# Kernel tuning notes

Hardware: AMD Instinct MI355X
Metric: run time of the kernel (lower is better)

The kernel has to match this reference:

```python
import jax, jax.numpy as jnp
import numpy as np

B, L, K, S, D, H, C = 32, 256, 50, 16, 128, 4, 128
V, NN, NU, NS = 50000, 100000, 50000, 5000


def mha(q, k, v, in_w, in_b, out_w, out_b, n_heads):
    # PyTorch nn.MultiheadAttention (batch_first, eval mode) semantics.
    d = q.shape[-1]
    hd = d // n_heads
    wq, wk, wv = jnp.split(in_w, 3, axis=0)
    bq, bk, bv = jnp.split(in_b, 3)
    def heads(t):
        return t.reshape(t.shape[:-1] + (n_heads, hd))
    qh = heads(q @ wq.T + bq)
    kh = heads(k @ wk.T + bk)
    vh = heads(v @ wv.T + bv)
    scores = jnp.einsum('...qhd,...khd->...hqk', qh, kh) / jnp.sqrt(jnp.asarray(hd, q.dtype))
    attn = jax.nn.softmax(scores, axis=-1)
    o = jnp.einsum('...hqk,...khd->...qhd', attn, vh)
    o = o.reshape(o.shape[:-2] + (d,))
    return o @ out_w.T + out_b


def conv1d(x, w, b):
    # x: [B, D, L], w: [Cout, D, k]
    y = jax.lax.conv_general_dilated(x, w, (1,), 'VALID', dimension_numbers=('NCH', 'OIH', 'NCH'))
    return y + b[None, :, None]


def meta_path_module(paths, gru_wih, gru_whh, gru_bih, gru_bhh, in_w, in_b, out_w, out_b, ln_g, ln_b):
    # paths: [B, S, T, D] -> [B, D]
    b, s, t, d = paths.shape
    x = paths.reshape(b * s, t, d)
    def step(h, xt):
        gi = xt @ gru_wih.T + gru_bih
        gh = h @ gru_whh.T + gru_bhh
        ir, iz, inn = jnp.split(gi, 3, axis=-1)
        hr, hz, hn = jnp.split(gh, 3, axis=-1)
        r = jax.nn.sigmoid(ir + hr)
        z = jax.nn.sigmoid(iz + hz)
        n = jnp.tanh(inn + r * hn)
        return (1.0 - z) * n + z * h, None
    h0 = jnp.zeros((b * s, d), paths.dtype)
    h, _ = jax.lax.scan(step, h0, jnp.swapaxes(x, 0, 1))
    enc = h.reshape(b, s, d)
    attn = mha(enc, enc, enc, in_w, in_b, out_w, out_b, H)
    y = enc + attn
    mu = jnp.mean(y, -1, keepdims=True)
    var = jnp.var(y, -1, keepdims=True)
    y = (y - mu) / jnp.sqrt(var + 1e-5) * ln_g + ln_b
    return jnp.mean(y, axis=1)


def _forward(word_table, news_table, user_table, source_table,
             wa_in_w, wa_in_b, wa_out_w, wa_out_b,
             conv_w3, conv_b3, conv_w4, conv_b4, conv_w5, conv_b5, fc_w, fc_b,
             nsn_gru_wih, nsn_gru_whh, nsn_gru_bih, nsn_gru_bhh,
             nsn_in_w, nsn_in_b, nsn_out_w, nsn_out_b, nsn_ln_g, nsn_ln_b,
             nun_gru_wih, nun_gru_whh, nun_gru_bih, nun_gru_bhh,
             nun_in_w, nun_in_b, nun_out_w, nun_out_b, nun_ln_g, nun_ln_b,
             mp_w1, mp_b1, mp_w2, mp_b2, cls_w1, cls_b1, cls_w2, cls_b2,
             news_ids, news_word_indices, word_ctx_ids, nsn_src, nsn_end, nun_usr, nun_end):
    # --- fine-grained word embeds: per-token query attending over context news ---
    base = word_table[news_word_indices]              # [B, L, D]
    ctx = news_table[word_ctx_ids]                    # [B, L, K, D] (dominant gather)
    q = base[:, :, None, :]                           # [B, L, 1, D]
    fine = mha(q, ctx, ctx, wa_in_w, wa_in_b, wa_out_w, wa_out_b, H)[:, :, 0, :]
    pad = (news_word_indices == 0)[..., None]
    doc = jnp.where(pad, jnp.zeros((), base.dtype), fine)   # padding_idx=0 -> zeros
    # --- coarse CNN encoder ---
    x = jnp.swapaxes(doc, 1, 2)                       # [B, D, L]
    pooled = [jnp.max(jax.nn.relu(conv1d(x, w, b)), axis=2)
              for w, b in ((conv_w3, conv_b3), (conv_w4, conv_b4), (conv_w5, conv_b5))]
    semantic = jnp.concatenate(pooled, axis=1) @ fc_w.T + fc_b   # [B, D]
    # --- meta-path interaction ---
    start = jnp.broadcast_to(news_table[news_ids][:, None, :], (B, S, D))
    nsn_paths = jnp.stack([start, source_table[nsn_src], news_table[nsn_end]], axis=2)
    nun_paths = jnp.stack([start, user_table[nun_usr], news_table[nun_end]], axis=2)
    nsn_e = meta_path_module(nsn_paths, nsn_gru_wih, nsn_gru_whh, nsn_gru_bih, nsn_gru_bhh,
                             nsn_in_w, nsn_in_b, nsn_out_w, nsn_out_b, nsn_ln_g, nsn_ln_b)
    nun_e = meta_path_module(nun_paths, nun_gru_wih, nun_gru_whh, nun_gru_bih, nun_gru_bhh,
                             nun_in_w, nun_in_b, nun_out_w, nun_out_b, nun_ln_g, nun_ln_b)
    stack = jnp.stack([nsn_e, nun_e], axis=1)         # [B, 2, D]
    sc = jnp.tanh(stack @ mp_w1.T + mp_b1) @ mp_w2.T + mp_b2
    w = jax.nn.softmax(sc, axis=1)
    struct = jnp.sum(stack * w, axis=1)
    comb = jnp.concatenate([semantic, struct], axis=1)
    hcls = jax.nn.relu(comb @ cls_w1.T + cls_b1)
    return hcls @ cls_w2.T + cls_b2                   # [B, 2]


def setup_inputs() -> dict:
    key = jax.random.key(0)
    ks = iter(jax.random.split(key, 80))
    def p(shape):
        return (jax.random.normal(next(ks), shape, jnp.float32) * 0.02)
    inp = {}
    inp['news_ids'] = jax.random.randint(next(ks), (B,), 0, NN)
    inp['news_word_indices'] = jax.random.randint(next(ks), (B, L), 0, V)
    inp['word_ctx_ids'] = jax.random.randint(next(ks), (B, L, K), 0, NN)
    inp['nsn_src'] = jax.random.randint(next(ks), (B, S), 0, NS)
    inp['nsn_end'] = jax.random.randint(next(ks), (B, S), 0, NN)
    inp['nun_usr'] = jax.random.randint(next(ks), (B, S), 0, NU)
    inp['nun_end'] = jax.random.randint(next(ks), (B, S), 0, NN)
    inp['word_table'] = p((V, D)).at[0].set(0.0)
    inp['news_table'] = p((NN, D))
    inp['user_table'] = p((NU, D))
    inp['source_table'] = p((NS, D))
    inp['wa_in_w'] = p((3 * D, D)); inp['wa_in_b'] = p((3 * D,))
    inp['wa_out_w'] = p((D, D)); inp['wa_out_b'] = p((D,))
    for k in (3, 4, 5):
        inp[f'conv_w{k}'] = p((C, D, k)); inp[f'conv_b{k}'] = p((C,))
    inp['fc_w'] = p((D, 3 * C)); inp['fc_b'] = p((D,))
    for pre in ('nsn', 'nun'):
        inp[f'{pre}_gru_wih'] = p((3 * D, D)); inp[f'{pre}_gru_whh'] = p((3 * D, D))
        inp[f'{pre}_gru_bih'] = p((3 * D,)); inp[f'{pre}_gru_bhh'] = p((3 * D,))
        inp[f'{pre}_in_w'] = p((3 * D, D)); inp[f'{pre}_in_b'] = p((3 * D,))
        inp[f'{pre}_out_w'] = p((D, D)); inp[f'{pre}_out_b'] = p((D,))
        inp[f'{pre}_ln_g'] = jnp.ones((D,), jnp.float32); inp[f'{pre}_ln_b'] = jnp.zeros((D,), jnp.float32)
    inp['mp_w1'] = p((D // 2, D)); inp['mp_b1'] = p((D // 2,))
    inp['mp_w2'] = p((1, D // 2)); inp['mp_b2'] = p((1,))
    inp['cls_w1'] = p((D, 2 * D)); inp['cls_b1'] = p((D,))
    inp['cls_w2'] = p((2, D)); inp['cls_b2'] = p((2,))
    return inp


def reference(word_table, news_table, user_table, source_table,
              wa_in_w, wa_in_b, wa_out_w, wa_out_b,
              conv_w3, conv_b3, conv_w4, conv_b4, conv_w5, conv_b5, fc_w, fc_b,
              nsn_gru_wih, nsn_gru_whh, nsn_gru_bih, nsn_gru_bhh,
              nsn_in_w, nsn_in_b, nsn_out_w, nsn_out_b, nsn_ln_g, nsn_ln_b,
              nun_gru_wih, nun_gru_whh, nun_gru_bih, nun_gru_bhh,
              nun_in_w, nun_in_b, nun_out_w, nun_out_b, nun_ln_g, nun_ln_b,
              mp_w1, mp_b1, mp_w2, mp_b2, cls_w1, cls_b1, cls_w2, cls_b2,
              news_ids, news_word_indices, word_ctx_ids, nsn_src, nsn_end, nun_usr, nun_end):
    return _forward(word_table, news_table, user_table, source_table,
                    wa_in_w, wa_in_b, wa_out_w, wa_out_b,
                    conv_w3, conv_b3, conv_w4, conv_b4, conv_w5, conv_b5, fc_w, fc_b,
                    nsn_gru_wih, nsn_gru_whh, nsn_gru_bih, nsn_gru_bhh,
                    nsn_in_w, nsn_in_b, nsn_out_w, nsn_out_b, nsn_ln_g, nsn_ln_b,
                    nun_gru_wih, nun_gru_whh, nun_gru_bih, nun_gru_bhh,
                    nun_in_w, nun_in_b, nun_out_w, nun_out_b, nun_ln_g, nun_ln_b,
                    mp_w1, mp_b1, mp_w2, mp_b2, cls_w1, cls_b1, cls_w2, cls_b2,
                    news_ids, news_word_indices, word_ctx_ids, nsn_src, nsn_end, nun_usr, nun_end)
```

## Files before the change

### kernel.cpp

```cpp
#include <hip/hip_runtime.h>
#include <hip/hip_bf16.h>

#define BB 32
#define LL 256
#define KC 50
#define SS 16
#define DD 128
#define NH 4
#define CC 128
#define VV 50000
#define NNN 100000
#define NUU 50000
#define NSS 5000

typedef __attribute__((ext_vector_type(8))) short bf16x8;
typedef __attribute__((ext_vector_type(8))) unsigned short u16x8;
typedef __attribute__((ext_vector_type(4))) float f32x4;

#define APAD 132

__device__ __forceinline__ float dot4(float4 a, float4 b){
  return a.x*b.x + a.y*b.y + a.z*b.z + a.w*b.w;
}

__device__ __forceinline__ unsigned short f2bf(float f){
  union { float f; unsigned int u; } v; v.f = f;
  unsigned int r = (v.u + 0x7FFFu + ((v.u >> 16) & 1u)) >> 16;
  return (unsigned short)r;
}
__device__ __forceinline__ float bf2f(unsigned short s){
  union { unsigned int u; float f; } v; v.u = ((unsigned int)s) << 16;
  return v.f;
}

__global__ __launch_bounds__(256) void k_prep(
    const float* __restrict__ w3, const float* __restrict__ w4,
    const float* __restrict__ w5,
    const float* __restrict__ wih0, const float* __restrict__ whh0,
    const float* __restrict__ wih1, const float* __restrict__ whh1,
    const float* __restrict__ in_w, const float* __restrict__ out_w,
    unsigned short* __restrict__ wb3, unsigned short* __restrict__ wb4,
    unsigned short* __restrict__ wb5, unsigned short* __restrict__ wgb,
    unsigned short* __restrict__ wab){
  int e = blockIdx.x*256 + threadIdx.x;
  if (e < CC*DD*3){ int c=e/(DD*3), rm=e%(DD*3), d=rm/3, jj=rm%3;
    wb3[((size_t)jj*CC + c)*DD + d] = f2bf(w3[e]); }
  if (e < CC*DD*4){ int c=e/(DD*4), rm=e%(DD*4), d=rm/4, jj=rm%4;
    wb4[((size_t)jj*CC + c)*DD + d] = f2bf(w4[e]); }
  if (e < CC*DD*5){ int c=e/(DD*5), rm=e%(DD*5), d=rm/5, jj=rm%5;
    wb5[((size_t)jj*CC + c)*DD + d] = f2bf(w5[e]); }
  if (e < 384*DD){
    wgb[e]          = f2bf(wih0[e]);
    wgb[49152 + e]  = f2bf(whh0[e]);
    wgb[98304 + e]  = f2bf(wih1[e]);
    wgb[147456 + e] = f2bf(whh1[e]);
    wab[e]          = f2bf(in_w[e]);
  }
  if (e >= 384*DD && e < 512*DD) wab[e] = f2bf(out_w[e - 384*DD]);
}

__global__ __launch_bounds__(256) void k_projkv(
    const float* __restrict__ news, const unsigned short* __restrict__ wkvb,
    const float* __restrict__ in_b, unsigned short* __restrict__ nK,
    unsigned short* __restrict__ nV){
  __shared__ __align__(16) unsigned short Ts[64*APAD];
  const int tid = threadIdx.x;
  const int r0 = blockIdx.x * 64;
  for (int i = tid; i < 64*32; i += 256){
    int row = i >> 5, j = i & 31;
    int gr = r0 + row;
    float4 v = (gr < NNN) ? ((const float4*)(news + (size_t)gr*DD))[j]
                          : make_float4(0.f,0.f,0.f,0.f);
    unsigned short* d = Ts + row*APAD + j*4;
    d[0]=f2bf(v.x); d[1]=f2bf(v.y); d[2]=f2bf(v.z); d[3]=f2bf(v.w);
  }
  __syncthreads();
  const int wave = tid >> 6;
  const int lane = tid & 63;
  const int l15  = lane & 15;
  const int quad = lane >> 4;
  bf16x8 afr[4][4];
  #pragma unroll
  for (int mt=0; mt<4; mt++)
    #pragma unroll
    for (int ks=0; ks<4; ks++)
      afr[mt][ks] = *(const bf16x8*)(Ts + (mt*16 + l15)*APAD + ks*32 + quad*8);
  __syncthreads();
  for (int pass=0; pass<2; pass++){
    unsigned short* outp = pass ? nV : nK;
    #pragma unroll
    for (int t=0; t<2; t++){
      const int n0 = wave*32 + t*16;
      bf16x8 bfr[4];
      #pragma unroll
      for (int ks=0; ks<4; ks++)
        bfr[ks] = *(const bf16x8*)(wkvb + (size_t)(pass*128 + n0 + l15)*DD + ks*32 + quad*8);
      const float bias = in_b[128 + pass*128 + n0 + l15];
      #pragma unroll
      for (int mt=0; mt<4; mt++){
        f32x4 acc = {0.f,0.f,0.f,0.f};
        #pragma unroll
        for (int ks=0; ks<4; ks++)
          acc = __builtin_amdgcn_mfma_f32_16x16x32_bf16(afr[mt][ks], bfr[ks], acc, 0,0,0);
        const int col = n0 + l15;
        const int rb  = mt*16 + quad*4;
        #pragma unroll
        for (int r=0;r<4;r++)
          Ts[(rb + r)*APAD + col] = f2bf(acc[r] + bias);
      }
    }
    __syncthreads();
    for (int c = tid; c < 64*32; c += 256){
      int row = c >> 5, col4 = (c & 31) * 4;
      int gr = r0 + row;
      if (gr < NNN)
        *(unsigned long long*)(outp + (size_t)gr*128 + col4) =
            *(const unsigned long long*)(Ts + row*APAD + col4);
    }
    __syncthreads();
  }
}

__global__ __launch_bounds__(256) void k_qh(
    const float* __restrict__ word_table, const int* __restrict__ widx,
    const unsigned short* __restrict__ wqb, const float* __restrict__ in_b,
    float* __restrict__ qh){
  __shared__ __align__(16) unsigned short As[64*APAD];
  __shared__ int idx[64];
  const int tid = threadIdx.x;
  const int p0 = blockIdx.x * 64;
  if (tid < 64) idx[tid] = widx[p0 + tid];
  __syncthreads();
  for (int i = tid; i < 64*32; i += 256){
    int row = i >> 5, j = i & 31;
    float4 v = ((const float4*)(word_table + (size_t)idx[row]*DD))[j];
    unsigned short* d = As + row*APAD + j*4;
    d[0]=f2bf(v.x); d[1]=f2bf(v.y); d[2]=f2bf(v.z); d[3]=f2bf(v.w);
  }
  __syncthreads();
  const int wave = tid >> 6;
  const int lane = tid & 63;
  const int l15  = lane & 15;
  const int quad = lane >> 4;
  bf16x8 afr[4][4];
  #pragma unroll
  for (int mt=0; mt<4; mt++)
    #pragma unroll
    for (int ks=0; ks<4; ks++)
      afr[mt][ks] = *(const bf16x8*)(As + (mt*16 + l15)*APAD + ks*32 + quad*8);
  #pragma unroll
  for (int nt=0; nt<2; nt++){
    const int n0 = wave*32 + nt*16;
    bf16x8 bfr[4];
    #pragma unroll
    for (int ks=0; ks<4; ks++)
      bfr[ks] = *(const bf16x8*)(wqb + (size_t)(n0+l15)*DD + ks*32 + quad*8);
    const float bias = in_b[n0 + l15];
    #pragma unroll
    for (int mt=0; mt<4; mt++){
      f32x4 acc = {0.f,0.f,0.f,0.f};
      #pragma unroll
      for (int ks=0; ks<4; ks++)
        acc = __builtin_amdgcn_mfma_f32_16x16x32_bf16(afr[mt][ks], bfr[ks], acc, 0,0,0);
      #pragma unroll
      for (int r=0;r<4;r++){
        int m = mt*16 + quad*4 + r;
        qh[(size_t)(p0+m)*DD + n0 + l15] = acc[r] + bias;
      }
    }
  }
}

__global__ __launch_bounds__(64) void k_attn(
    const float* __restrict__ qh, const unsigned short* __restrict__ nK,
    const unsigned short* __restrict__ nV, const int* __restrict__ ctx_ids,
    float* __restrict__ o_out){
  const int p = blockIdx.x;
  const int lane = threadIdx.x;
  const int r = lane >> 4;
  const int g = lane & 15;
  const int h = g >> 2;
  __shared__ int ids[52];
  __shared__ float sc[NH][52];
  if (lane < KC) ids[lane] = ctx_ids[(size_t)p*KC + lane];
  float qv[8];
  {
    const float4* qp = (const float4*)(qh + (size_t)p*DD + g*8);
    float4 q0 = qp[0], q1 = qp[1];
    qv[0]=q0.x; qv[1]=q0.y; qv[2]=q0.z; qv[3]=q0.w;
    qv[4]=q1.x; qv[5]=q1.y; qv[6]=q1.z; qv[7]=q1.w;
  }
  __syncthreads();
  for (int kb=0; kb<13; kb++){
    int k2 = kb*4 + r;
    int row = ids[(k2 < KC) ? k2 : 0];
    u16x8 kv = *(const u16x8*)(nK + (size_t)row*DD + g*8);
    float pr = 0.f;
    #pragma unroll
    for (int j=0;j<8;j++) pr += qv[j]*bf2f(kv[j]);
    pr += __shfl_xor(pr, 1, 64);
    pr += __shfl_xor(pr, 2, 64);
    if ((g & 3) == 0 && k2 < KC) sc[h][k2] = pr;
  }
  __syncthreads();
  {
    const int hh = lane >> 4, kc = lane & 15;
    const float scale = 0.17677669529663687f;
    float mx = -1e30f;
    #pragma unroll
    for (int q4=0;q4<4;q4++){ int k2=kc+q4*16; if (k2<KC) mx = fmaxf(mx, sc[hh][k2]); }
    mx = fmaxf(mx, __shfl_xor(mx, 1, 64));
    mx = fmaxf(mx, __shfl_xor(mx, 2, 64));
    mx = fmaxf(mx, __shfl_xor(mx, 4, 64));
    mx = fmaxf(mx, __shfl_xor(mx, 8, 64));
    float sm = 0.f;
    float ev[4];
    #pragma unroll
    for (int q4=0;q4<4;q4++){
      int k2=kc+q4*16;
      ev[q4] = (k2<KC) ? __expf((sc[hh][k2]-mx)*scale) : 0.f;
      sm += ev[q4];
    }
    sm += __shfl_xor(sm, 1, 64);
    sm += __shfl_xor(sm, 2, 64);
    sm += __shfl_xor(sm, 4, 64);
    sm += __shfl_xor(sm, 8, 64);
    float inv = 1.f/sm;
    #pragma unroll
    for (int q4=0;q4<4;q4++){ int k2=kc+q4*16; if (k2<KC) sc[hh][k2] = ev[q4]*inv; }
  }
  __syncthreads();
  float acc[8];
  #pragma unroll
  for (int j=0;j<8;j++) acc[j]=0.f;
  for (int kb=0; kb<13; kb++){
    int k2 = kb*4 + r;
    int row = ids[(k2 < KC) ? k2 : 0];
    float w = (k2 < KC) ? sc[h][k2] : 0.f;
    u16x8 vv = *(const u16x8*)(nV + (size_t)row*DD + g*8);
    #pragma unroll
    for (int j=0;j<8;j++) acc[j] += w*bf2f(vv[j]);
  }
  #pragma unroll
  for (int j=0;j<8;j++){
    acc[j] += __shfl_xor(acc[j], 16, 64);
    acc[j] += __shfl_xor(acc[j], 32, 64);
  }
  if (r == 0){
    float4* op = (float4*)(o_out + (size_t)p*DD + g*8);
    op[0] = make_float4(acc[0],acc[1],acc[2],acc[3]);
    op[1] = make_float4(acc[4],acc[5],acc[6],acc[7]);
  }
}

__global__ __launch_bounds__(256) void k_wo(
    const float* __restrict__ o_attn, const int* __restrict__ widx,
    const unsigned short* __restrict__ wob, const float* __restrict__ out_b,
    float* __restrict__ doc){
  __shared__ __align__(16) unsigned short As[64*APAD];
  __shared__ int wm[64];
  const int tid = threadIdx.x;
  const int p0 = blockIdx.x * 64;
  if (tid < 64) wm[tid] = widx[p0 + tid];
  for (int i = tid; i < 64*32; i += 256){
    int row = i >> 5, j = i & 31;
    float4 v = ((const float4*)(o_attn + (size_t)(p0+row)*DD))[j];
    unsigned short* d = As + row*APAD + j*4;
    d[0]=f2bf(v.x); d[1]=f2bf(v.y); d[2]=f2bf(v.z); d[3]=f2bf(v.w);
  }
  __syncthreads();
  const int wave = tid >> 6;
  const int lane = tid & 63;
  const int l15  = lane & 15;
  const int quad = lane >> 4;
  bf16x8 afr[4][4];
  #pragma unroll
  for (int mt=0; mt<4; mt++)
    #pragma unroll
    for (int ks=0; ks<4; ks++)
      afr[mt][ks] = *(const bf16x8*)(As + (mt*16 + l15)*APAD + ks*32 + quad*8);
  #pragma unroll
  for (int nt=0; nt<2; nt++){
    const int n0 = wave*32 + nt*16;
    bf16x8 bfr[4];
    #pragma unroll
    for (int ks=0; ks<4; ks++)
      bfr[ks] = *(const bf16x8*)(wob + (size_t)(n0+l15)*DD + ks*32 + quad*8);
    const float bias = out_b[n0 + l15];
    #pragma unroll
    for (int mt=0; mt<4; mt++){
      f32x4 acc = {0.f,0.f,0.f,0.f};
      #pragma unroll
      for (int ks=0; ks<4; ks++)
        acc = __builtin_amdgcn_mfma_f32_16x16x32_bf16(afr[mt][ks], bfr[ks], acc, 0,0,0);
      #pragma unroll
      for (int r=0;r<4;r++){
        int m = mt*16 + quad*4 + r;
        doc[(size_t)(p0+m)*DD + n0 + l15] = (wm[m] == 0) ? 0.0f : (acc[r] + bias);
      }
    }
  }
}

#define CROWS 68
#define CPAD 136
__global__ __launch_bounds__(256) void k_conv(
    const float* __restrict__ doc, const unsigned short* __restrict__ wb3,
    const unsigned short* __restrict__ wb4, const unsigned short* __restrict__ wb5,
    float* __restrict__ convp){
  __shared__ __align__(16) char smem[CROWS*CPAD*2];
  unsigned short* ds = (unsigned short*)smem;
  float* smf = (float*)smem;
  const int blk = blockIdx.x;
  const int chunk = blk & 3;
  const int j = (blk >> 2) % 3;
  const int b = blk / 12;
  const int kk = 3 + j;
  const int T = LL - kk + 1;
  const int t0 = chunk * 64;
  const int nrows = 64 + kk - 1;
  const unsigned short* wb = (j==0) ? wb3 : (j==1) ? wb4 : wb5;
  const int tid = threadIdx.x;
  for (int i = tid; i < nrows*32; i += 256){
    int row = i >> 5, q4 = i & 31;
    int gt = t0 + row;
    float4 v = (gt < LL) ? ((const float4*)(doc + ((size_t)b*LL + gt)*DD))[q4]
                         : make_float4(0.f,0.f,0.f,0.f);
    unsigned short* dp = ds + row*CPAD + q4*4;
    dp[0]=f2bf(v.x); dp[1]=f2bf(v.y); dp[2]=f2bf(v.z); dp[3]=f2bf(v.w);
  }
  __syncthreads();
  const int wave = tid >> 6;
  const int lane = tid & 63;
  const int l15  = lane & 15;
  const int quad = lane >> 4;
  f32x4 acc[8];
  #pragma unroll
  for (int nt=0;nt<8;nt++) acc[nt] = (f32x4){0.f,0.f,0.f,0.f};
  for (int jj=0; jj<kk; jj++){
    #pragma unroll
    for (int ks=0; ks<4; ks++){
      bf16x8 af = *(const bf16x8*)(ds + (wave*16 + l15 + jj)*CPAD + ks*32 + quad*8);
      #pragma unroll
      for (int nt=0; nt<8; nt++){
        bf16x8 bf = *(const bf16x8*)(wb + ((size_t)jj*CC + nt*16 + l15)*DD + ks*32 + quad*8);
        acc[nt] = __builtin_amdgcn_mfma_f32_16x16x32_bf16(af, bf, acc[nt], 0,0,0);
      }
    }
  }
  __syncthreads();
  #pragma unroll
  for (int nt=0; nt<8; nt++){
    float mx = -1e30f;
    #pragma unroll
    for (int r=0;r<4;r++){
      int t = t0 + wave*16 + quad*4 + r;
      mx = fmaxf(mx, (t < T) ? acc[nt][r] : -1e30f);
    }
    mx = fmaxf(mx, __shfl_xor(mx, 16, 64));
    mx = fmaxf(mx, __shfl_xor(mx, 32, 64));
    if (quad == 0) smf[wave*128 + nt*16 + l15] = mx;
  }
  __syncthreads();
  if (tid < 128){
    float m4 = fmaxf(fmaxf(smf[tid], smf[128+tid]), fmaxf(smf[256+tid], smf[384+tid]));
    convp[(((size_t)b*3 + j)*4 + chunk)*CC + tid] = m4;
  }
}

#define GSTR 392
__global__ __launch_bounds__(256) void k_gru(
    const float* __restrict__ news_table, const float* __restrict__ user_table,
    const float* __restrict__ source_table,
    const int* __restrict__ news_ids, const int* __restrict__ nsn_src,
    const int* __restrict__ nsn_end, const int* __restrict__ nun_usr,
    const int* __restrict__ nun_end,
    const unsigned short* __restrict__ wgb,
    const float* __restrict__ bih0, const float* __restrict__ bhh0,
    const float* __restrict__ bih1, const float* __restrict__ bhh1,
    float* __restrict__ enc){
  __shared__ __align__(16) unsigned short xs[16][CPAD];
  __shared__ __align__(16) unsigned short hs[16][CPAD];
  __shared__ float hf[8][128];
  __shared__ float gi[8][GSTR];
  __shared__ float gh[8][GSTR];
  const int blk = blockIdx.x;
  const int m  = blk >> 6;
  const int b  = (blk >> 1) & 31;
  const int s0 = (blk & 1) * 8;
  const int tid = threadIdx.x;
  const int wave = tid >> 6, lane = tid & 63, l15 = lane & 15, quad = lane >> 4;
  const unsigned short* Wih = wgb + (size_t)m*2*384*DD;
  const unsigned short* Whh = Wih + 384*DD;
  const float* bih = m ? bih1 : bih0;
  const float* bhh = m ? bhh1 : bhh0;
  for (int i=tid;i<16*CPAD;i+=256){ (&xs[0][0])[i]=0; (&hs[0][0])[i]=0; }
  for (int i=tid;i<8*128;i+=256) (&hf[0][0])[i]=0.f;
  __syncthreads();
  for (int t=0;t<3;t++){
    {
      int s = tid >> 5, j = tid & 31;
      int row; const float* tab;
      if (t==0){ row = news_ids[b]; tab = news_table; }
      else if (t==1){ row = m ? nun_usr[b*SS+s0+s] : nsn_src[b*SS+s0+s];
                      tab = m ? user_table : source_table; }
      else { row = m ? nun_end[b*SS+s0+s] : nsn_end[b*SS+s0+s]; tab = news_table; }
      float4 v = ((const float4*)(tab + (size_t)row*DD))[j];
      unsigned short* dp = &xs[s][j*4];
      dp[0]=f2bf(v.x); dp[1]=f2bf(v.y); dp[2]=f2bf(v.z); dp[3]=f2bf(v.w);
    }
    __syncthreads();
    bf16x8 ax[4], ah[4];
    #pragma unroll
    for (int ks=0;ks<4;ks++){
      ax[ks] = *(const bf16x8*)&xs[l15][ks*32+quad*8];
      ah[ks] = *(const bf16x8*)&hs[l15][ks*32+quad*8];
    }
    #pragma unroll
    for (int nt=0;nt<6;nt++){
      const int n0 = wave*96 + nt*16;
      f32x4 ga = {0.f,0.f,0.f,0.f}, ha = {0.f,0.f,0.f,0.f};
      #pragma unroll
      for (int ks=0;ks<4;ks++){
        bf16x8 bi = *(const bf16x8*)(Wih + (size_t)(n0+l15)*DD + ks*32+quad*8);
        ga = __builtin_amdgcn_mfma_f32_16x16x32_bf16(ax[ks], bi, ga, 0,0,0);
        bf16x8 bh = *(const bf16x8*)(Whh + (size_t)(n0+l15)*DD + ks*32+quad*8);
        ha = __builtin_amdgcn_mfma_f32_16x16x32_bf16(ah[ks], bh, ha, 0,0,0);
      }
      if (quad < 2){
        #pragma unroll
        for (int r=0;r<4;r++){
          gi[quad*4+r][n0+l15] = ga[r];
          gh[quad*4+r][n0+l15] = ha[r];
        }
      }
    }
    __syncthreads();
    #pragma unroll
    for (int k=0;k<4;k++){
      int it = tid + k*256;
      int s = it >> 7, g = it & 127;
      float rr = 1.f/(1.f+__expf(-(gi[s][g] + gh[s][g] + bih[g] + bhh[g])));
      float zz = 1.f/(1.f+__expf(-(gi[s][128+g] + gh[s][128+g] + bih[128+g] + bhh[128+g])));
      float nn = tanhf(gi[s][256+g] + bih[256+g] + rr*(gh[s][256+g] + bhh[256+g]));
      float hnew = (1.f-zz)*nn + zz*hf[s][g];
      hf[s][g] = hnew;
      hs[s][g] = f2bf(hnew);
    }
    __syncthreads();
  }
  {
    int s = tid >> 5, j = tid & 31;
    float4 v = ((const float4*)hf[s])[j];
    ((float4*)(enc + (((size_t)m*BB + b)*SS + (s0+s))*DD))[j] = v;
  }
}

__global__ __launch_bounds__(128, 2) void k_metamha(
    const float* __restrict__ enc,
    const float* __restrict__ inw0, const float* __restrict__ inb0,
    const float* __restrict__ outw0, const float* __restrict__ outb0,
    const float* __restrict__ lng0, const float* __restrict__ lnb0,
    const float* __restrict__ inw1, const float* __restrict__ inb1,
    const float* __restrict__ outw1, const float* __restrict__ outb1,
    const float* __restrict__ lng1, const float* __restrict__ lnb1,
    float* __restrict__ meta_e){
  const int m = blockIdx.x >> 5;
  const int b = blockIdx.x & 31;
  const int c = threadIdx.x;
  const float* in_w  = m?inw1:inw0;  const float* in_b  = m?inb1:inb0;
  const float* out_w = m?outw1:outw0; const float* out_b = m?outb1:outb0;
  const float* lng   = m?lng1:lng0;  const float* lnb   = m?lnb1:lnb0;
  __shared__ float e[16][128], q[16][128], k[16][128], v[16][128];
  __shared__ float at[4][16][16];
  __shared__ float mu[16], rs[16];
  const float* esrc = enc + ((size_t)m*BB + b)*SS*DD;
  for (int i=c;i<16*128;i+=128) ((float*)e)[i] = esrc[i];
  __syncthreads();
  {
    float aq[16], ak[16], av[16];
    float bq = in_b[c], bk = in_b[128+c], bv = in_b[256+c];
    #pragma unroll
    for (int s=0;s<16;s++){ aq[s]=bq; ak[s]=bk; av[s]=bv; }
    const float4* wq4 = (const float4*)(in_w + c*DD);
    const float4* wk4 = (const float4*)(in_w + (128+c)*DD);
    const float4* wv4 = (const float4*)(in_w + (256+c)*DD);
    for (int j=0;j<32;j++){
      float4 a0=wq4[j], a1=wk4[j], a2=wv4[j];
      #pragma unroll
      for (int s=0;s<16;s++){
        float4 ev = ((const float4*)e[s])[j];
        aq[s]+=dot4(a0,ev); ak[s]+=dot4(a1,ev); av[s]+=dot4(a2,ev);
      }
    }
    #pragma unroll
    for (int s=0;s<16;s++){ q[s][c]=aq[s]; k[s][c]=ak[s]; v[s][c]=av[s]; }
  }
  __syncthreads();
  for (int r=0;r<8;r++){
    int lin = r*128 + c;
    int h = lin >> 8, qi = (lin>>4)&15, ki = lin&15;
    float sum=0.f;
    const float* qp = &q[qi][h*32];
    const float* kp = &k[ki][h*32];
    for (int x=0;x<32;x++) sum += qp[x]*kp[x];
    at[h][qi][ki] = sum * 0.17677669529663687f;
  }
  __syncthreads();
  if (c < 64){
    int h = c>>4, qi = c&15;
    float mx=-1e30f;
    for (int ki=0;ki<16;ki++) mx = fmaxf(mx, at[h][qi][ki]);
    float sm=0.f;
    for (int ki=0;ki<16;ki++){ float ee=__expf(at[h][qi][ki]-mx); at[h][qi][ki]=ee; sm+=ee; }
    float inv=1.f/sm;
    for (int ki=0;ki<16;ki++) at[h][qi][ki]*=inv;
  }
  __syncthreads();
  {
    int h = c>>5;
    float o[16];
    #pragma unroll
    for (int s=0;s<16;s++){
      float acc=0.f;
      for (int ki=0;ki<16;ki++) acc += at[h][s][ki]*v[ki][c];
      o[s]=acc;
    }
    __syncthreads();
    #pragma unroll
    for (int s=0;s<16;s++) q[s][c]=o[s];
  }
  __syncthreads();
  {
    float ay[16];
    float bo = out_b[c];
    #pragma unroll
    for (int s=0;s<16;s++) ay[s] = bo + e[s][c];
    const float4* wo4 = (const float4*)(out_w + c*DD);
    for (int j=0;j<32;j++){
      float4 wv_ = wo4[j];
      #pragma unroll
      for (int s=0;s<16;s++) ay[s] += dot4(wv_, ((const float4*)q[s])[j]);
    }
    __syncthreads();
    #pragma unroll
    for (int s=0;s<16;s++) e[s][c] = ay[s];
  }
  __syncthreads();
  if (c < 16){
    float sm=0.f;
    for (int d=0;d<128;d++) sm += e[c][d];
    float mean = sm*(1.f/128.f);
    float vs=0.f;
    for (int d=0;d<128;d++){ float df = e[c][d]-mean; vs += df*df; }
    mu[c]=mean; rs[c]=rsqrtf(vs*(1.f/128.f) + 1e-5f);
  }
  __syncthreads();
  {
    float g = lng[c], bb2 = lnb[c];
    float acc=0.f;
    #pragma unroll
    for (int s=0;s<16;s++) acc += (e[s][c]-mu[s])*rs[s]*g + bb2;
    meta_e[((size_t)m*BB+b)*DD + c] = acc * (1.f/16.f);
  }
}

__global__ __launch_bounds__(128) void k_final(
    const float* __restrict__ convp,
    const float* __restrict__ cb3, const float* __restrict__ cb4,
    const float* __restrict__ cb5,
    const float* __restrict__ fc_w, const float* __restrict__ fc_b,
    const float* __restrict__ meta_e,
    const float* __restrict__ mp_w1, const float* __restrict__ mp_b1,
    const float* __restrict__ mp_w2, const float* __restrict__ mp_b2,
    const float* __restrict__ cls_w1, const float* __restrict__ cls_b1,
    const float* __restrict__ cls_w2, const float* __restrict__ cls_b2,
    float* __restrict__ out){
  const int b = blockIdx.x;
  const int c = threadIdx.x;
  __shared__ float pooled[384];
  __shared__ float comb[256];
  __shared__ float hcls[128];
  __shared__ float tt[2][64];
  __shared__ float wsc[2];
  for (int idx=c; idx<384; idx+=128){
    int j = idx >> 7, cc2 = idx & 127;
    const float* base = convp + (((size_t)b*3 + j)*4)*CC + cc2;
    float mx = -1e30f;
    for (int ci=0;ci<4;ci++) mx = fmaxf(mx, base[ci*CC]);
    const float* cb = (j==0)?cb3:(j==1)?cb4:cb5;
    pooled[idx] = fmaxf(mx + cb[cc2], 0.f);
  }
  __syncthreads();
  {
    float acc = fc_b[c];
    const float* wr = fc_w + (size_t)c*384;
    for (int i=0;i<384;i++) acc += pooled[i]*wr[i];
    comb[c] = acc;
  }
  if (c < 64){
    for (int m=0;m<2;m++){
      const float* ev = meta_e + ((size_t)m*BB+b)*DD;
      float acc = mp_b1[c];
      const float* wr = mp_w1 + (size_t)c*DD;
      for (int i=0;i<DD;i++) acc += ev[i]*wr[i];
      tt[m][c] = tanhf(acc);
    }
  }
  __syncthreads();
  if (c == 0){
    float s0 = mp_b2[0], s1 = mp_b2[0];
    for (int j=0;j<64;j++){ s0 += tt[0][j]*mp_w2[j]; s1 += tt[1][j]*mp_w2[j]; }
    float mx = fmaxf(s0,s1);
    float e0 = __expf(s0-mx), e1 = __expf(s1-mx);
    wsc[0] = e0/(e0+e1); wsc[1] = e1/(e0+e1);
  }
  __syncthreads();
  comb[128+c] = wsc[0]*meta_e[((size_t)b)*DD + c]
              + wsc[1]*meta_e[((size_t)(BB+b))*DD + c];
  __syncthreads();
  {
    float acc = cls_b1[c];
    const float* wr = cls_w1 + (size_t)c*256;
    for (int i=0;i<256;i++) acc += comb[i]*wr[i];
    hcls[c] = fmaxf(acc, 0.f);
  }
  __syncthreads();
  if (c < 2){
    float acc = cls_b2[c];
    const float* wr = cls_w2 + (size_t)c*DD;
    for (int i=0;i<DD;i++) acc += hcls[i]*wr[i];
    out[b*2 + c] = acc;
  }
}

extern "C" void kernel_launch(void* const* d_in, const int* in_sizes, int n_in,
                              void* d_out, int out_size, void* d_ws, size_t ws_size,
                              hipStream_t stream){
  const int* news_ids = (const int*)d_in[0];
  const int* nwi      = (const int*)d_in[1];
  const int* ctx_ids  = (const int*)d_in[2];
  const int* nsn_src  = (const int*)d_in[3];
  const int* nsn_end  = (const int*)d_in[4];
  const int* nun_usr  = (const int*)d_in[5];
  const int* nun_end  = (const int*)d_in[6];
  const float* word_table   = (const float*)d_in[7];
  const float* news_table   = (const float*)d_in[8];
  const float* user_table   = (const float*)d_in[9];
  const float* source_table = (const float*)d_in[10];
  const float* wa_in_w  = (const float*)d_in[11];
  const float* wa_in_b  = (const float*)d_in[12];
  const float* wa_out_w = (const float*)d_in[13];
  const float* wa_out_b = (const float*)d_in[14];
  const float* conv_w3 = (const float*)d_in[15];
  const float* conv_b3 = (const float*)d_in[16];
  const float* conv_w4 = (const float*)d_in[17];
  const float* conv_b4 = (const float*)d_in[18];
  const float* conv_w5 = (const float*)d_in[19];
  const float* conv_b5 = (const float*)d_in[20];
  const float* fc_w = (const float*)d_in[21];
  const float* fc_b = (const float*)d_in[22];
  const float* wih0 = (const float*)d_in[23];
  const float* whh0 = (const float*)d_in[24];
  const float* bih0 = (const float*)d_in[25];
  const float* bhh0 = (const float*)d_in[26];
  const float* inw0 = (const float*)d_in[27];
  const float* inb0 = (const float*)d_in[28];
  const float* outw0 = (const float*)d_in[29];
  const float* outb0 = (const float*)d_in[30];
  const float* lng0 = (const float*)d_in[31];
  const float* lnb0 = (const float*)d_in[32];
  const float* wih1 = (const float*)d_in[33];
  const float* whh1 = (const float*)d_in[34];
  const float* bih1 = (const float*)d_in[35];
  const float* bhh1 = (const float*)d_in[36];
  const float* inw1 = (const float*)d_in[37];
  const float* inb1 = (const float*)d_in[38];
  const float* outw1 = (const float*)d_in[39];
  const float* outb1 = (const float*)d_in[40];
  const float* lng1 = (const float*)d_in[41];
  const float* lnb1 = (const float*)d_in[42];
  const float* mp_w1 = (const float*)d_in[43];
  const float* mp_b1 = (const float*)d_in[44];
  const float* mp_w2 = (const float*)d_in[45];
  const float* mp_b2 = (const float*)d_in[46];
  const float* cls_w1 = (const float*)d_in[47];
  const float* cls_b1 = (const float*)d_in[48];
  const float* cls_w2 = (const float*)d_in[49];
  const float* cls_b2 = (const float*)d_in[50];

  char* wsb = (char*)d_ws;
  unsigned short* nK = (unsigned short*)wsb;
  unsigned short* nV = nK + (size_t)NNN*DD;
  unsigned short* wb3 = nV + (size_t)NNN*DD;
  unsigned short* wb4 = wb3 + (size_t)CC*DD*3;
  unsigned short* wb5 = wb4 + (size_t)CC*DD*4;
  unsigned short* wgb = wb5 + (size_t)CC*DD*5;
  unsigned short* wab = wgb + (size_t)4*384*DD;
  float* qh     = (float*)(wab + (size_t)512*DD);
  float* o_at   = qh + (size_t)BB*LL*DD;
  float* doc    = o_at + (size_t)BB*LL*DD;
  float* convp  = doc + (size_t)BB*LL*DD;
  float* enc    = convp + BB*3*4*CC;
  float* meta_e = enc + (size_t)2*BB*SS*DD;
  const size_t need_bytes = (size_t)((char*)(meta_e + 2*BB*DD) - wsb);
  if (ws_size < need_bytes) return;

  const unsigned short* wqb  = wab;
  const unsigned short* wkvb = wab + (size_t)128*DD;
  const unsigned short* wob  = wab + (size_t)384*DD;

  k_prep<<<dim3(320), dim3(256), 0, stream>>>(conv_w3, conv_w4, conv_w5,
      wih0, whh0, wih1, whh1, wa_in_w, wa_out_w, wb3, wb4, wb5, wgb, wab);
  k_projkv<<<dim3((NNN+63)/64), dim3(256), 0, stream>>>(news_table, wkvb, wa_in_b, nK, nV);
  k_qh<<<dim3(BB*LL/64), dim3(256), 0, stream>>>(word_table, nwi, wqb, wa_in_b, qh);
  k_attn<<<dim3(BB*LL), dim3(64), 0, stream>>>(qh, nK, nV, ctx_ids, o_at);
  k_wo<<<dim3(BB*LL/64), dim3(256), 0, stream>>>(o_at, nwi, wob, wa_out_b, doc);
  k_conv<<<dim3(BB*3*4), dim3(256), 0, stream>>>(doc, wb3, wb4, wb5, convp);
  k_gru<<<dim3(128), dim3(256), 0, stream>>>(news_table, user_table, source_table,
      news_ids, nsn_src, nsn_end, nun_usr, nun_end,
      wgb, bih0, bhh0, bih1, bhh1, enc);
  k_metamha<<<dim3(64), dim3(128), 0, stream>>>(enc,
      inw0, inb0, outw0, outb0, lng0, lnb0,
      inw1, inb1, outw1, outb1, lng1, lnb1, meta_e);
  k_final<<<dim3(BB), dim3(128), 0, stream>>>(convp, conv_b3, conv_b4, conv_b5,
      fc_w, fc_b, meta_e, mp_w1, mp_b1, mp_w2, mp_b2,
      cls_w1, cls_b1, cls_w2, cls_b2, (float*)d_out);
}
```

Before: 396.7 us.

## Store attention and doc intermediates as bf16 and shrink qh/wo GEMM blocks

The attention output and the masked doc projection are now written as bf16 instead of fp32. This halves their global traffic, and the consuming kernels (k_wo, k_conv) load the bf16 values directly without converting. k_qh and k_wo become single-wavefront blocks of 16 rows that load their A fragments straight from global memory into registers, removing the shared-memory staging and block barriers. The smaller blocks mean more launches and more repeated weight-fragment loads per row, and precision is unchanged because the values were already rounded to bf16 before the MFMA.

```diff
diff --git a/kernel.cpp b/kernel.cpp
--- a/kernel.cpp
+++ b/kernel.cpp
@@ -121,52 +121,41 @@
   }
 }
 
-__global__ __launch_bounds__(256) void k_qh(
+__global__ __launch_bounds__(64) void k_qh(
     const float* __restrict__ word_table, const int* __restrict__ widx,
     const unsigned short* __restrict__ wqb, const float* __restrict__ in_b,
     float* __restrict__ qh){
-  __shared__ __align__(16) unsigned short As[64*APAD];
-  __shared__ int idx[64];
-  const int tid = threadIdx.x;
-  const int p0 = blockIdx.x * 64;
-  if (tid < 64) idx[tid] = widx[p0 + tid];
-  __syncthreads();
-  for (int i = tid; i < 64*32; i += 256){
-    int row = i >> 5, j = i & 31;
-    float4 v = ((const float4*)(word_table + (size_t)idx[row]*DD))[j];
-    unsigned short* d = As + row*APAD + j*4;
-    d[0]=f2bf(v.x); d[1]=f2bf(v.y); d[2]=f2bf(v.z); d[3]=f2bf(v.w);
-  }
-  __syncthreads();
-  const int wave = tid >> 6;
-  const int lane = tid & 63;
-  const int l15  = lane & 15;
-  const int quad = lane >> 4;
-  bf16x8 afr[4][4];
-  #pragma unroll
-  for (int mt=0; mt<4; mt++)
-    #pragma unroll
-    for (int ks=0; ks<4; ks++)
-      afr[mt][ks] = *(const bf16x8*)(As + (mt*16 + l15)*APAD + ks*32 + quad*8);
-  #pragma unroll
-  for (int nt=0; nt<2; nt++){
-    const int n0 = wave*32 + nt*16;
+  const int lane = threadIdx.x;
+  const int l15 = lane & 15, quad = lane >> 4;
+  const int p0 = blockIdx.x * 16;
+  const int row = widx[p0 + l15];
+  const float* src = word_table + (size_t)row*DD + quad*8;
+  bf16x8 afr[4];
+  #pragma unroll
+  for (int ks=0; ks<4; ks++){
+    float4 v0 = *(const float4*)(src + ks*32);
+    float4 v1 = *(const float4*)(src + ks*32 + 4);
+    bf16x8 a;
+    a[0]=(short)f2bf(v0.x); a[1]=(short)f2bf(v0.y); a[2]=(short)f2bf(v0.z); a[3]=(short)f2bf(v0.w);
+    a[4]=(short)f2bf(v1.x); a[5]=(short)f2bf(v1.y); a[6]=(short)f2bf(v1.z); a[7]=(short)f2bf(v1.w);
+    afr[ks] = a;
+  }
+  #pragma unroll
+  for (int nt=0; nt<8; nt++){
+    const int n0 = nt*16;
     bf16x8 bfr[4];
     #pragma unroll
     for (int ks=0; ks<4; ks++)
       bfr[ks] = *(const bf16x8*)(wqb + (size_t)(n0+l15)*DD + ks*32 + quad*8);
     const float bias = in_b[n0 + l15];
-    #pragma unroll
-    for (int mt=0; mt<4; mt++){
-      f32x4 acc = {0.f,0.f,0.f,0.f};
-      #pragma unroll
-      for (int ks=0; ks<4; ks++)
-        acc = __builtin_amdgcn_mfma_f32_16x16x32_bf16(afr[mt][ks], bfr[ks], acc, 0,0,0);
-      #pragma unroll
-      for (int r=0;r<4;r++){
-        int m = mt*16 + quad*4 + r;
-        qh[(size_t)(p0+m)*DD + n0 + l15] = acc[r] + bias;
-      }
+    f32x4 acc = {0.f,0.f,0.f,0.f};
+    #pragma unroll
+    for (int ks=0; ks<4; ks++)
+      acc = __builtin_amdgcn_mfma_f32_16x16x32_bf16(afr[ks], bfr[ks], acc, 0,0,0);
+    #pragma unroll
+    for (int r=0;r<4;r++){
+      int m = quad*4 + r;
+      qh[(size_t)(p0+m)*DD + n0 + l15] = acc[r] + bias;
     }
   }
 }
@@ -174,7 +163,7 @@
 __global__ __launch_bounds__(64) void k_attn(
     const float* __restrict__ qh, const unsigned short* __restrict__ nK,
     const unsigned short* __restrict__ nV, const int* __restrict__ ctx_ids,
-    float* __restrict__ o_out){
+    unsigned short* __restrict__ o_out){
   const int p = blockIdx.x;
   const int lane = threadIdx.x;
   const int r = lane >> 4;
@@ -247,57 +236,44 @@
     acc[j] += __shfl_xor(acc[j], 32, 64);
   }
   if (r == 0){
-    float4* op = (float4*)(o_out + (size_t)p*DD + g*8);
-    op[0] = make_float4(acc[0],acc[1],acc[2],acc[3]);
-    op[1] = make_float4(acc[4],acc[5],acc[6],acc[7]);
-  }
-}
-
-__global__ __launch_bounds__(256) void k_wo(
-    const float* __restrict__ o_attn, const int* __restrict__ widx,
+    u16x8 o;
+    #pragma unroll
+    for (int j=0;j<8;j++) o[j] = f2bf(acc[j]);
+    *(u16x8*)(o_out + (size_t)p*DD + g*8) = o;
+  }
+}
+
+__global__ __launch_bounds__(64) void k_wo(
+    const unsigned short* __restrict__ o_attn, const int* __restrict__ widx,
     const unsigned short* __restrict__ wob, const float* __restrict__ out_b,
-    float* __restrict__ doc){
-  __shared__ __align__(16) unsigned short As[64*APAD];
-  __shared__ int wm[64];
-  const int tid = threadIdx.x;
-  const int p0 = blockIdx.x * 64;
-  if (tid < 64) wm[tid] = widx[p0 + tid];
-  for (int i = tid; i < 64*32; i += 256){
-    int row = i >> 5, j = i & 31;
-    float4 v = ((const float4*)(o_attn + (size_t)(p0+row)*DD))[j];
-    unsigned short* d = As + row*APAD + j*4;
-    d[0]=f2bf(v.x); d[1]=f2bf(v.y); d[2]=f2bf(v.z); d[3]=f2bf(v.w);
-  }
-  __syncthreads();
-  const int wave = tid >> 6;
-  const int lane = tid & 63;
-  const int l15  = lane & 15;
-  const int quad = lane >> 4;
-  bf16x8 afr[4][4];
-  #pragma unroll
-  for (int mt=0; mt<4; mt++)
-    #pragma unroll
-    for (int ks=0; ks<4; ks++)
-      afr[mt][ks] = *(const bf16x8*)(As + (mt*16 + l15)*APAD + ks*32 + quad*8);
-  #pragma unroll
-  for (int nt=0; nt<2; nt++){
-    const int n0 = wave*32 + nt*16;
+    unsigned short* __restrict__ doc){
+  const int lane = threadIdx.x;
+  const int l15 = lane & 15, quad = lane >> 4;
+  const int p0 = blockIdx.x * 16;
+  bf16x8 afr[4];
+  #pragma unroll
+  for (int ks=0; ks<4; ks++)
+    afr[ks] = *(const bf16x8*)(o_attn + (size_t)(p0+l15)*DD + ks*32 + quad*8);
+  int msk[4];
+  #pragma unroll
+  for (int r=0;r<4;r++) msk[r] = widx[p0 + quad*4 + r];
+  #pragma unroll
+  for (int nt=0; nt<8; nt++){
+    const int n0 = nt*16;
     bf16x8 bfr[4];
     #pragma unroll
     for (int ks=0; ks<4; ks++)
       bfr[ks] = *(const bf16x8*)(wob + (size_t)(n0+l15)*DD + ks*32 + quad*8);
     const float bias = out_b[n0 + l15];
-    #pragma unroll
-    for (int mt=0; mt<4; mt++){
-      f32x4 acc = {0.f,0.f,0.f,0.f};
-      #pragma unroll
-      for (int ks=0; ks<4; ks++)
-        acc = __builtin_amdgcn_mfma_f32_16x16x32_bf16(afr[mt][ks], bfr[ks], acc, 0,0,0);
-      #pragma unroll
-      for (int r=0;r<4;r++){
-        int m = mt*16 + quad*4 + r;
-        doc[(size_t)(p0+m)*DD + n0 + l15] = (wm[m] == 0) ? 0.0f : (acc[r] + bias);
-      }
+    f32x4 acc = {0.f,0.f,0.f,0.f};
+    #pragma unroll
+    for (int ks=0; ks<4; ks++)
+      acc = __builtin_amdgcn_mfma_f32_16x16x32_bf16(afr[ks], bfr[ks], acc, 0,0,0);
+    #pragma unroll
+    for (int r=0;r<4;r++){
+      int m = quad*4 + r;
+      doc[(size_t)(p0+m)*DD + n0 + l15] = (msk[r] == 0) ? (unsigned short)0
+                                                        : f2bf(acc[r] + bias);
     }
   }
 }
@@ -305,7 +281,7 @@
 #define CROWS 68
 #define CPAD 136
 __global__ __launch_bounds__(256) void k_conv(
-    const float* __restrict__ doc, const unsigned short* __restrict__ wb3,
+    const unsigned short* __restrict__ doc, const unsigned short* __restrict__ wb3,
     const unsigned short* __restrict__ wb4, const unsigned short* __restrict__ wb5,
     float* __restrict__ convp){
   __shared__ __align__(16) char smem[CROWS*CPAD*2];
@@ -321,13 +297,12 @@
   const int nrows = 64 + kk - 1;
   const unsigned short* wb = (j==0) ? wb3 : (j==1) ? wb4 : wb5;
   const int tid = threadIdx.x;
-  for (int i = tid; i < nrows*32; i += 256){
-    int row = i >> 5, q4 = i & 31;
+  for (int i = tid; i < nrows*16; i += 256){
+    int row = i >> 4, q8 = i & 15;
     int gt = t0 + row;
-    float4 v = (gt < LL) ? ((const float4*)(doc + ((size_t)b*LL + gt)*DD))[q4]
-                         : make_float4(0.f,0.f,0.f,0.f);
-    unsigned short* dp = ds + row*CPAD + q4*4;
-    dp[0]=f2bf(v.x); dp[1]=f2bf(v.y); dp[2]=f2bf(v.z); dp[3]=f2bf(v.w);
+    u16x8 v = (u16x8){0,0,0,0,0,0,0,0};
+    if (gt < LL) v = *(const u16x8*)(doc + ((size_t)b*LL + gt)*DD + q8*8);
+    *(u16x8*)(ds + row*CPAD + q8*8) = v;
   }
   __syncthreads();
   const int wave = tid >> 6;
@@ -698,9 +673,9 @@
   unsigned short* wgb = wb5 + (size_t)CC*DD*5;
   unsigned short* wab = wgb + (size_t)4*384*DD;
   float* qh     = (float*)(wab + (size_t)512*DD);
-  float* o_at   = qh + (size_t)BB*LL*DD;
-  float* doc    = o_at + (size_t)BB*LL*DD;
-  float* convp  = doc + (size_t)BB*LL*DD;
+  unsigned short* o_at = (unsigned short*)(qh + (size_t)BB*LL*DD);
+  unsigned short* doc  = (unsigned short*)((float*)o_at + (size_t)BB*LL*DD);
+  float* convp  = (float*)doc + (size_t)BB*LL*DD;
   float* enc    = convp + BB*3*4*CC;
   float* meta_e = enc + (size_t)2*BB*SS*DD;
   const size_t need_bytes = (size_t)((char*)(meta_e + 2*BB*DD) - wsb);
@@ -713,9 +688,9 @@
   k_prep<<<dim3(320), dim3(256), 0, stream>>>(conv_w3, conv_w4, conv_w5,
       wih0, whh0, wih1, whh1, wa_in_w, wa_out_w, wb3, wb4, wb5, wgb, wab);
   k_projkv<<<dim3((NNN+63)/64), dim3(256), 0, stream>>>(news_table, wkvb, wa_in_b, nK, nV);
-  k_qh<<<dim3(BB*LL/64), dim3(256), 0, stream>>>(word_table, nwi, wqb, wa_in_b, qh);
+  k_qh<<<dim3(BB*LL/16), dim3(64), 0, stream>>>(word_table, nwi, wqb, wa_in_b, qh);
   k_attn<<<dim3(BB*LL), dim3(64), 0, stream>>>(qh, nK, nV, ctx_ids, o_at);
-  k_wo<<<dim3(BB*LL/64), dim3(256), 0, stream>>>(o_at, nwi, wob, wa_out_b, doc);
+  k_wo<<<dim3(BB*LL/16), dim3(64), 0, stream>>>(o_at, nwi, wob, wa_out_b, doc);
   k_conv<<<dim3(BB*3*4), dim3(256), 0, stream>>>(doc, wb3, wb4, wb5, convp);
   k_gru<<<dim3(128), dim3(256), 0, stream>>>(news_table, user_table, source_table,
       news_ids, nsn_src, nsn_end, nun_usr, nun_end,
```

Result: faster. 385.7 us (-2.8%).
